# Kernel optimization log

Hardware: AMD Instinct MI355X
Metric: run time of the kernel (lower is better)

The kernel has to match this reference:

```python
import jax, jax.numpy as jnp
import numpy as np


def setup_inputs() -> dict:
    key = jax.random.key(0)
    ks = jax.random.split(key, 12)
    L, B, T, E, H = 8, 256, 8, 1024, 1024
    w_scale = 1.0 / np.sqrt(E + H)  # keep gates out of saturation (mimics Linear init scale)
    inp = {
        "x": jax.random.normal(ks[0], (B, T, E), dtype=jnp.float32),
        "h0": jax.random.normal(ks[1], (L, B, H), dtype=jnp.float32),
        "c0": jax.random.normal(ks[2], (L, B, H), dtype=jnp.float32),
        "Wu": jax.random.normal(ks[3], (L, E + H, H), dtype=jnp.float32) * w_scale,
        "bu": jax.random.normal(ks[4], (L, H), dtype=jnp.float32) * w_scale,
        "Wf": jax.random.normal(ks[5], (L, E + H, H), dtype=jnp.float32) * w_scale,
        "bf": jax.random.normal(ks[6], (L, H), dtype=jnp.float32) * w_scale,
        "Wo": jax.random.normal(ks[7], (L, E + H, H), dtype=jnp.float32) * w_scale,
        "bo": jax.random.normal(ks[8], (L, H), dtype=jnp.float32) * w_scale,
        "Wc": jax.random.normal(ks[9], (L, E + H, H), dtype=jnp.float32) * w_scale,
        "bc": jax.random.normal(ks[10], (L, H), dtype=jnp.float32) * w_scale,
    }
    return inp


def reference(x, h0, c0, Wu, bu, Wf, bf, Wo, bo, Wc, bc):
    # x: [B,T,E]; h0,c0: [L,B,H]; W*: [L,E+H,H]; b*: [L,H]
    # Faithful to source: num_cells layers, time loop over first num_cells steps (T == L here).
    L = h0.shape[0]
    h = jnp.transpose(h0, (1, 0, 2))  # [B,L,H]
    c = jnp.transpose(c0, (1, 0, 2))

    def step(carry, xt):  # xt: [B,E]
        h, c = carry
        inp = xt
        hs, cs = [], []
        for l in range(L):
            zh = jnp.concatenate([inp, h[:, l]], axis=-1)  # [B, E+H]
            u = jax.nn.sigmoid(zh @ Wu[l] + bu[l])
            f = jax.nn.sigmoid(zh @ Wf[l] + bf[l])
            o = jax.nn.sigmoid(zh @ Wo[l] + bo[l])
            c_tilde = jnp.tanh(zh @ Wc[l] + bc[l])
            c_new = f * c[:, l] + u * c_tilde
            h_new = o * jnp.tanh(c_new)
            hs.append(h_new)
            cs.append(c_new)
            inp = h_new
        h = jnp.stack(hs, axis=1)
        c = jnp.stack(cs, axis=1)
        return (h, c), (h_new, c_new)  # emit top-layer h_t, c_t

    (_, _), (hs, cs) = jax.lax.scan(step, (h, c), jnp.transpose(x, (1, 0, 2)))
    hidden_states = jnp.transpose(hs, (1, 0, 2))  # [B,T,H]
    memory_states = jnp.transpose(cs, (1, 0, 2))
    h_t = hidden_states[:, -1:, :]  # [B,1,H], matches torch slice-shape
    c_t = memory_states[:, -1:, :]
    return hidden_states, memory_states, h_t, c_t
```

## Files before the change

kernel.cpp:

```cpp
#include <hip/hip_runtime.h>
#include <hip/hip_bf16.h>

#define B_ 256
#define T_ 8
#define E_ 1024
#define H_ 1024
#define L_ 8
#define KD 2048
#define ND 4096

#define BM 256
#define BN 128
#define BK 64
#define ABYTES 32768
#define BUFBYTES 49152

typedef __bf16 bf16x8 __attribute__((ext_vector_type(8)));
typedef float floatx4 __attribute__((ext_vector_type(4)));

struct bh4 { __hip_bfloat16 x, y, z, w; };

__device__ __forceinline__ float sigm(float x) { return 1.f / (1.f + __expf(-x)); }
__device__ __forceinline__ float tanh_(float x) { return 1.f - 2.f / (__expf(2.f * x) + 1.f); }

__device__ __forceinline__ void async16(const void* g, void* l) {
    __builtin_amdgcn_global_load_lds(
        (const __attribute__((address_space(1))) void*)g,
        (__attribute__((address_space(3))) void*)l, 16, 0, 0);
}

__global__ __launch_bounds__(256) void prep_weights(
    const float* __restrict__ Wu, const float* __restrict__ Wf,
    const float* __restrict__ Wo, const float* __restrict__ Wc,
    __hip_bfloat16* __restrict__ WT)
{
    __shared__ float sm[32][33];
    int bid = blockIdx.x;
    int jt = bid & 31;
    int kt = (bid >> 5) & 63;
    int g  = (bid >> 11) & 3;
    int l  = bid >> 13;
    const float* src = (g == 0) ? Wu : (g == 1) ? Wf : (g == 2) ? Wo : Wc;
    int tid = threadIdx.x;
    int jl = tid & 31;
    int kl0 = tid >> 5;
#pragma unroll
    for (int r = 0; r < 4; ++r) {
        int kl = r * 8 + kl0;
        sm[kl][jl] = src[((size_t)(l * KD + kt * 32 + kl)) * 1024 + jt * 32 + jl];
    }
    __syncthreads();
    int jw = tid >> 3;
    int kc = (tid & 7) * 4;
    bh4 v;
    v.x = __float2bfloat16(sm[kc + 0][jw]);
    v.y = __float2bfloat16(sm[kc + 1][jw]);
    v.z = __float2bfloat16(sm[kc + 2][jw]);
    v.w = __float2bfloat16(sm[kc + 3][jw]);
    size_t n = (size_t)(jt * 32 + jw) * 4 + g;
    *(bh4*)&WT[((size_t)l * ND + n) * KD + kt * 32 + kc] = v;
}

__global__ __launch_bounds__(256) void prep_misc(
    const float* __restrict__ x,  const float* __restrict__ h0,
    const float* __restrict__ c0,
    const float* __restrict__ bu, const float* __restrict__ bfv,
    const float* __restrict__ bo, const float* __restrict__ bc,
    __hip_bfloat16* __restrict__ xbf, __hip_bfloat16* __restrict__ hb0,
    float* __restrict__ cbuf, float* __restrict__ bcat)
{
    size_t i = (size_t)blockIdx.x * 256 + threadIdx.x;
    const size_t NX = (size_t)B_ * T_ * E_;
    const size_t NH = (size_t)L_ * B_ * H_;
    if (i < NX) {
        xbf[i] = __float2bfloat16(x[i]);
    } else if (i < NX + NH) {
        size_t j = i - NX; hb0[j] = __float2bfloat16(h0[j]);
    } else if (i < NX + 2 * NH) {
        size_t j = i - NX - NH; cbuf[j] = c0[j];
    } else if (i < NX + 2 * NH + (size_t)L_ * ND) {
        size_t j = i - NX - 2 * NH;
        int l = (int)(j >> 12); int n = (int)(j & 4095);
        int jj = n >> 2; int g = n & 3;
        const float* bs = (g == 0) ? bu : (g == 1) ? bfv : (g == 2) ? bo : bc;
        bcat[j] = bs[l * 1024 + jj];
    }
}

__global__ __launch_bounds__(512) void lstm_step(
    int d, int tmin,
    const __hip_bfloat16* __restrict__ xbf,
    const __hip_bfloat16* __restrict__ WT,
    const float* __restrict__ bcat,
    __hip_bfloat16* __restrict__ hb0,
    __hip_bfloat16* __restrict__ hb1,
    float* __restrict__ cbuf,
    float* __restrict__ out)
{
    __shared__ __align__(16) char smraw[2][BUFBYTES];

    int cell = blockIdx.x >> 5;
    int nb   = blockIdx.x & 31;
    int t = tmin + cell;
    int l = d - t;

    const __hip_bfloat16* hread  = (t & 1) ? hb1 : hb0;
    __hip_bfloat16*       hwrite = (t & 1) ? hb0 : hb1;

    const __hip_bfloat16* A1; int sA1;
    if (l == 0) { A1 = xbf + (size_t)t * E_;               sA1 = T_ * E_; }
    else        { A1 = hwrite + (size_t)(l - 1) * B_ * H_; sA1 = H_; }
    const __hip_bfloat16* A2 = hread + (size_t)l * B_ * H_;
    const __hip_bfloat16* Bbase = WT + ((size_t)l * ND + (size_t)nb * BN) * KD;

    int tid  = threadIdx.x;
    int lane = tid & 63;
    int wid  = tid >> 6;
    int wm = (wid & 3) * 64;
    int wn = (wid >> 2) * 64;
    int lr   = lane & 15;
    int quad = lane >> 4;

    int srow = tid >> 3;
    int c    = (tid & 7) ^ (srow & 7);
    const __hip_bfloat16* pA1[4];
    const __hip_bfloat16* pA2[4];
    const __hip_bfloat16* pB[2];
#pragma unroll
    for (int s = 0; s < 4; ++s) {
        int row = s * 64 + srow;
        pA1[s] = A1 + (size_t)row * sA1 + c * 8;
        pA2[s] = A2 + (size_t)row * H_ + c * 8 - E_;
    }
#pragma unroll
    for (int s = 0; s < 2; ++s) {
        int row = s * 64 + srow;
        pB[s] = Bbase + (size_t)row * KD + c * 8;
    }
    int ldsWaveOff = wid * 1024;

    auto stage = [&](int k0, int buf) {
        char* dst = smraw[buf];
        bool first = (k0 < E_);
#pragma unroll
        for (int s = 0; s < 4; ++s) {
            const __hip_bfloat16* g = (first ? pA1[s] : pA2[s]) + k0;
            async16(g, dst + s * 8192 + ldsWaveOff);
        }
#pragma unroll
        for (int s = 0; s < 2; ++s) {
            async16(pB[s] + k0, dst + ABYTES + s * 8192 + ldsWaveOff);
        }
    };

    floatx4 acc[4][4];
    floatx4 zero = {0.f, 0.f, 0.f, 0.f};
#pragma unroll
    for (int mi = 0; mi < 4; ++mi)
#pragma unroll
        for (int ni = 0; ni < 4; ++ni) acc[mi][ni] = zero;

    stage(0, 0);
    __syncthreads();

    for (int kt = 0; kt < KD / BK; ++kt) {
        int cur = kt & 1;
        if (kt < KD / BK - 1) stage((kt + 1) * BK, cur ^ 1);

        const __hip_bfloat16* sm = (const __hip_bfloat16*)smraw[cur];
        const __hip_bfloat16* smB = sm + ABYTES / 2;
#pragma unroll
        for (int ks = 0; ks < 2; ++ks) {
            int xo = (((ks * 4 + quad) ^ (lr & 7)) * 8);
            bf16x8 af[4], bfr[4];
#pragma unroll
            for (int mi = 0; mi < 4; ++mi)
                af[mi] = *(const bf16x8*)&sm[(wm + mi * 16 + lr) * 64 + xo];
#pragma unroll
            for (int ni = 0; ni < 4; ++ni)
                bfr[ni] = *(const bf16x8*)&smB[(wn + ni * 16 + lr) * 64 + xo];
#pragma unroll
            for (int mi = 0; mi < 4; ++mi)
#pragma unroll
                for (int ni = 0; ni < 4; ++ni)
                    acc[mi][ni] = __builtin_amdgcn_mfma_f32_16x16x32_bf16(
                        af[mi], bfr[ni], acc[mi][ni], 0, 0, 0);
        }
        __syncthreads();
    }

    float* outH  = out;
    float* outC  = out + (size_t)B_ * T_ * H_;
    float* outHt = out + 2 * (size_t)B_ * T_ * H_;
    float* outCt = outHt + (size_t)B_ * H_;
    auto sC = (float(*)[BN + 4])smraw[0];

    for (int q = 0; q < 4; ++q) {
        __syncthreads();
        if ((wid & 3) == q) {
#pragma unroll
            for (int mi = 0; mi < 4; ++mi)
#pragma unroll
                for (int ni = 0; ni < 4; ++ni)
#pragma unroll
                    for (int r = 0; r < 4; ++r)
                        sC[mi * 16 + quad * 4 + r][wn + ni * 16 + lr] = acc[mi][ni][r];
        }
        __syncthreads();
#pragma unroll
        for (int s = 0; s < 4; ++s) {
            int p = tid + s * 512;
            int r  = p >> 5;
            int jj = p & 31;
            float4 v  = *(float4*)&sC[r][jj * 4];
            float4 bb = *(const float4*)&bcat[(size_t)l * ND + nb * BN + jj * 4];
            float u  = sigm(v.x + bb.x);
            float f  = sigm(v.y + bb.y);
            float o  = sigm(v.z + bb.z);
            float ct = tanh_(v.w + bb.w);
            int b = q * 64 + r;
            int j = nb * 32 + jj;
            size_t ci = ((size_t)l * B_ + b) * H_ + j;
            float cn = f * cbuf[ci] + u * ct;
            cbuf[ci] = cn;
            float hn = o * tanh_(cn);
            hwrite[ci] = __float2bfloat16(hn);
            if (l == L_ - 1) {
                size_t oi = ((size_t)b * T_ + t) * H_ + j;
                outH[oi] = hn;
                outC[oi] = cn;
                if (t == T_ - 1) {
                    outHt[(size_t)b * H_ + j] = hn;
                    outCt[(size_t)b * H_ + j] = cn;
                }
            }
        }
    }
}

extern "C" void kernel_launch(void* const* d_in, const int* in_sizes, int n_in,
                              void* d_out, int out_size, void* d_ws, size_t ws_size,
                              hipStream_t stream)
{
    const float* x   = (const float*)d_in[0];
    const float* h0  = (const float*)d_in[1];
    const float* c0  = (const float*)d_in[2];
    const float* Wu  = (const float*)d_in[3];
    const float* bu  = (const float*)d_in[4];
    const float* Wf  = (const float*)d_in[5];
    const float* bfv = (const float*)d_in[6];
    const float* Wo  = (const float*)d_in[7];
    const float* bo  = (const float*)d_in[8];
    const float* Wc  = (const float*)d_in[9];
    const float* bc  = (const float*)d_in[10];
    float* out = (float*)d_out;

    char* ws = (char*)d_ws;
    __hip_bfloat16* WT   = (__hip_bfloat16*)(ws);
    float*          bcat = (float*)(ws + 134217728);
    __hip_bfloat16* xbf  = (__hip_bfloat16*)(ws + 134348800);
    __hip_bfloat16* hb0  = (__hip_bfloat16*)(ws + 138543104);
    __hip_bfloat16* hb1  = (__hip_bfloat16*)(ws + 142737408);
    float*          cbuf = (float*)(ws + 146931712);

    hipLaunchKernelGGL(prep_weights, dim3(65536), dim3(256), 0, stream,
                       Wu, Wf, Wo, Wc, WT);
    size_t n2 = (size_t)2097152 * 3 + (size_t)L_ * ND;
    hipLaunchKernelGGL(prep_misc, dim3((unsigned)((n2 + 255) / 256)), dim3(256), 0, stream,
                       x, h0, c0, bu, bfv, bo, bc, xbf, hb0, cbuf, bcat);

    for (int dg = 0; dg <= (T_ - 1) + (L_ - 1); ++dg) {
        int tmin = dg > L_ - 1 ? dg - (L_ - 1) : 0;
        int tmax = dg < T_ - 1 ? dg : T_ - 1;
        int nc = tmax - tmin + 1;
        hipLaunchKernelGGL(lstm_step, dim3(nc * 32), dim3(512), 0, stream,
                           dg, tmin, xbf, WT, bcat, hb0, hb1, cbuf, out);
    }
}
```

Baseline: 962.3 us.

## Triple-buffer LDS pipeline with explicit vmcnt waits and widen weight-prep tiles

The GEMM K-loop goes from double to triple buffering. Loads are issued three tiles ahead and tracked with explicit s_waitcnt vmcnt counts and raw s_barrier in place of __syncthreads. MFMA blocks are wrapped in s_setprio to favour math issue. The weight transpose/convert kernel now handles 64-row K tiles and writes 16-byte bf16x8 vectors, halving its block count. The cost is more LDS per block (144KB), which may reduce occupancy, and hand-set wait counts that must match the per-thread load count.

```diff
diff --git a/kernel.cpp b/kernel.cpp
--- a/kernel.cpp
+++ b/kernel.cpp
@@ -14,11 +14,10 @@
 #define BK 64
 #define ABYTES 32768
 #define BUFBYTES 49152
+#define NT (KD / BK)
 
 typedef __bf16 bf16x8 __attribute__((ext_vector_type(8)));
 typedef float floatx4 __attribute__((ext_vector_type(4)));
-
-struct bh4 { __hip_bfloat16 x, y, z, w; };
 
 __device__ __forceinline__ float sigm(float x) { return 1.f / (1.f + __expf(-x)); }
 __device__ __forceinline__ float tanh_(float x) { return 1.f - 2.f / (__expf(2.f * x) + 1.f); }
@@ -34,31 +33,30 @@
     const float* __restrict__ Wo, const float* __restrict__ Wc,
     __hip_bfloat16* __restrict__ WT)
 {
-    __shared__ float sm[32][33];
+    __shared__ float sm[64][33];
     int bid = blockIdx.x;
     int jt = bid & 31;
-    int kt = (bid >> 5) & 63;
-    int g  = (bid >> 11) & 3;
-    int l  = bid >> 13;
+    int kt = (bid >> 5) & 31;
+    int g  = (bid >> 10) & 3;
+    int l  = bid >> 12;
     const float* src = (g == 0) ? Wu : (g == 1) ? Wf : (g == 2) ? Wo : Wc;
     int tid = threadIdx.x;
     int jl = tid & 31;
     int kl0 = tid >> 5;
 #pragma unroll
-    for (int r = 0; r < 4; ++r) {
+    for (int r = 0; r < 8; ++r) {
         int kl = r * 8 + kl0;
-        sm[kl][jl] = src[((size_t)(l * KD + kt * 32 + kl)) * 1024 + jt * 32 + jl];
+        sm[kl][jl] = src[((size_t)(l * KD + kt * 64 + kl)) * 1024 + jt * 32 + jl];
     }
     __syncthreads();
     int jw = tid >> 3;
-    int kc = (tid & 7) * 4;
-    bh4 v;
-    v.x = __float2bfloat16(sm[kc + 0][jw]);
-    v.y = __float2bfloat16(sm[kc + 1][jw]);
-    v.z = __float2bfloat16(sm[kc + 2][jw]);
-    v.w = __float2bfloat16(sm[kc + 3][jw]);
+    int kc = (tid & 7) * 8;
+    bf16x8 v;
+#pragma unroll
+    for (int i = 0; i < 8; ++i)
+        v[i] = (__bf16)sm[kc + i][jw];
     size_t n = (size_t)(jt * 32 + jw) * 4 + g;
-    *(bh4*)&WT[((size_t)l * ND + n) * KD + kt * 32 + kc] = v;
+    *(bf16x8*)&WT[((size_t)l * ND + n) * KD + kt * 64 + kc] = v;
 }
 
 __global__ __launch_bounds__(256) void prep_misc(
@@ -97,7 +95,7 @@
     float* __restrict__ cbuf,
     float* __restrict__ out)
 {
-    __shared__ __align__(16) char smraw[2][BUFBYTES];
+    __shared__ __align__(16) char smraw[3][BUFBYTES];
 
     int cell = blockIdx.x >> 5;
     int nb   = blockIdx.x & 31;
@@ -160,15 +158,18 @@
 #pragma unroll
         for (int ni = 0; ni < 4; ++ni) acc[mi][ni] = zero;
 
-    stage(0, 0);
-    __syncthreads();
-
-    for (int kt = 0; kt < KD / BK; ++kt) {
-        int cur = kt & 1;
-        if (kt < KD / BK - 1) stage((kt + 1) * BK, cur ^ 1);
-
-        const __hip_bfloat16* sm = (const __hip_bfloat16*)smraw[cur];
+    stage(0 * BK, 0);
+    stage(1 * BK, 1);
+    stage(2 * BK, 2);
+    asm volatile("s_waitcnt vmcnt(12)" ::: "memory");
+    __builtin_amdgcn_sched_barrier(0);
+    __builtin_amdgcn_s_barrier();
+
+    for (int kt = 0; kt < NT; ++kt) {
+        int cur = kt % 3;
+        const __hip_bfloat16* sm  = (const __hip_bfloat16*)smraw[cur];
         const __hip_bfloat16* smB = sm + ABYTES / 2;
+
 #pragma unroll
         for (int ks = 0; ks < 2; ++ks) {
             int xo = (((ks * 4 + quad) ^ (lr & 7)) * 8);
@@ -179,14 +180,30 @@
 #pragma unroll
             for (int ni = 0; ni < 4; ++ni)
                 bfr[ni] = *(const bf16x8*)&smB[(wn + ni * 16 + lr) * 64 + xo];
+            asm volatile("s_waitcnt lgkmcnt(0)" ::: "memory");
+            __builtin_amdgcn_sched_barrier(0);
+            __builtin_amdgcn_s_setprio(1);
 #pragma unroll
             for (int mi = 0; mi < 4; ++mi)
 #pragma unroll
                 for (int ni = 0; ni < 4; ++ni)
                     acc[mi][ni] = __builtin_amdgcn_mfma_f32_16x16x32_bf16(
                         af[mi], bfr[ni], acc[mi][ni], 0, 0, 0);
-        }
-        __syncthreads();
+            __builtin_amdgcn_s_setprio(0);
+        }
+
+        __builtin_amdgcn_sched_barrier(0);
+        __builtin_amdgcn_s_barrier();
+
+        if (kt + 3 < NT) stage((kt + 3) * BK, cur);
+
+        if (kt < NT - 1) {
+            if (kt + 3 < NT)      { asm volatile("s_waitcnt vmcnt(12)" ::: "memory"); }
+            else if (kt + 2 < NT) { asm volatile("s_waitcnt vmcnt(6)"  ::: "memory"); }
+            else                  { asm volatile("s_waitcnt vmcnt(0)"  ::: "memory"); }
+            __builtin_amdgcn_sched_barrier(0);
+            __builtin_amdgcn_s_barrier();
+        }
     }
 
     float* outH  = out;
@@ -263,7 +280,7 @@
     __hip_bfloat16* hb1  = (__hip_bfloat16*)(ws + 142737408);
     float*          cbuf = (float*)(ws + 146931712);
 
-    hipLaunchKernelGGL(prep_weights, dim3(65536), dim3(256), 0, stream,
+    hipLaunchKernelGGL(prep_weights, dim3(32768), dim3(256), 0, stream,
                        Wu, Wf, Wo, Wc, WT);
     size_t n2 = (size_t)2097152 * 3 + (size_t)L_ * ND;
     hipLaunchKernelGGL(prep_misc, dim3((unsigned)((n2 + 255) / 256)), dim3(256), 0, stream,
```

Result: no change. 969.9 us (+0.8%).
